# Performance work log

Hardware: AMD Instinct MI355X
Metric: run time of the kernel (lower is better)

Reference implementation:

```python
import jax, jax.numpy as jnp
import numpy as np
from jax import lax

CONV_SIZE = 5
MORPH_SIZE = 5
TH1_INIT = 0.5
STEP = 0.0005
LO, HI = 0.84, 0.86


def _maxpool(a):
    p = MORPH_SIZE // 2
    return lax.reduce_window(
        a, -jnp.inf, lax.max,
        window_dimensions=(1, 1, MORPH_SIZE, MORPH_SIZE),
        window_strides=(1, 1, 1, 1),
        padding=[(0, 0), (0, 0), (p, p), (p, p)])


def setup_inputs() -> dict:
    key = jax.random.key(0)
    k1, _ = jax.random.split(key)
    x = jax.random.uniform(k1, (8, 4, 1024, 1024), dtype=jnp.float32)
    blur_k = jnp.full((1, 1, CONV_SIZE, CONV_SIZE), 1.0 / CONV_SIZE ** 2, dtype=jnp.float32)
    return {"x": x, "blur_k": blur_k}


def reference(x, blur_k):
    N, c, h, w = x.shape
    xi = x.reshape(N * c, 1, h, w)
    out = lax.conv_general_dilated(
        xi, blur_k, window_strides=(1, 1), padding='SAME',
        dimension_numbers=('NCHW', 'OIHW', 'NCHW')).reshape(N, c, h, w)

    # iterative mean-based threshold (quantile) search, same as the torch while-loops
    out_c = lax.stop_gradient(out)

    def frac_above(th):
        return jnp.mean(jnp.where(out_c > th, 1.0, 0.0))

    th = jnp.float32(TH1_INIT)
    th = lax.while_loop(lambda t: frac_above(t) < LO, lambda t: t - STEP, th)
    th = lax.while_loop(lambda t: frac_above(t) > HI, lambda t: t + STEP, th)

    thr = jnp.where(out > th, 1.0, 0.0)
    # morphological close: max-pool then min-pool (min = -maxpool(-x))
    closed = -_maxpool(-_maxpool(thr))
    return closed  # torch casts to float64; kept float32 (see notes)
```

## Files before the change

kernel.cpp:

```cpp
#include <hip/hip_runtime.h>


#define K_STEPS 1024
#define LO_COUNT 28185723u
#define R_TILE 8
#define PT_ROWS 16

#define OFF_HIST 4096
#define OFF_KQ   16384

__global__ void k_init(const float* __restrict__ bk, unsigned int* __restrict__ U,
                       unsigned int* __restrict__ hist) {
    __shared__ float Tsh[K_STEPS];
    int t = threadIdx.x;
    for (int i = t; i < K_STEPS + 1; i += 256) hist[i] = 0u;
    if (t == 0) {
        float th = 0.5f;
        for (int k = 0; k < K_STEPS; k++) { Tsh[k] = th; th = th - 0.0005f; }
    }
    __syncthreads();
    double c = (double)bk[0] * (1.0 / 8388608.0);
    for (int k = t; k < K_STEPS; k += 256) {
        double T = (double)Tsh[k];
        unsigned int u;
        if (T < 0.0) {
            u = 0u;
        } else {
            u = (unsigned int)(floor(T / c) + 1.0);
            while (u > 0u && (double)(u - 1u) * c > T) u--;
            while (!((double)u * c > T)) u++;
        }
        U[k] = u;
    }
}

__device__ __forceinline__ uint4 cvt4(float4 f) {
    return make_uint4((unsigned int)(f.x * 8388608.0f),
                      (unsigned int)(f.y * 8388608.0f),
                      (unsigned int)(f.z * 8388608.0f),
                      (unsigned int)(f.w * 8388608.0f));
}

__device__ __forceinline__ int find_ki(const unsigned int* __restrict__ Us,
                                       float U0f, unsigned int s) {
    float g = (U0f - (float)s) * 9.5367432e-6f;
    int lo = (int)g - 2;
    lo = max(0, min(1019, lo));
    unsigned int a0 = Us[lo], a1 = Us[lo + 1], a2 = Us[lo + 2], a3 = Us[lo + 3];
    return lo + (int)(s < a0) + (int)(s < a1) + (int)(s < a2) + (int)(s < a3);
}

__global__ __launch_bounds__(256, 4) void
k_pass1(const float4* __restrict__ x4, const unsigned int* __restrict__ Ug,
        unsigned int* __restrict__ hist, unsigned short* __restrict__ kq16) {
    __shared__ unsigned int Us[K_STEPS];
    __shared__ unsigned int lh[K_STEPS + 1];
    int tid = threadIdx.x;
    int p = blockIdx.y, y0 = blockIdx.x * R_TILE;
    for (int i = tid; i < K_STEPS; i += 256) Us[i] = Ug[i];
    for (int i = tid; i < K_STEPS + 1; i += 256) lh[i] = 0u;
    __syncthreads();
    float U0f = (float)Us[0];

    const float4* pf = x4 + (size_t)p * 262144;
    int tB = (tid < 255) ? tid + 1 : 0;
    const uint4 z4 = make_uint4(0u, 0u, 0u, 0u);

    uint4 A[5], B[5];
    #pragma unroll
    for (int i = 0; i < 5; i++) {
        int yy = y0 - 2 + i;
        int yc = min(max(yy, 0), 1023);
        float4 fa = pf[yc * 256 + tid];
        float4 fb = pf[yc * 256 + tB];
        bool v = (unsigned)yy < 1024u;
        A[i] = v ? cvt4(fa) : z4;
        B[i] = v ? cvt4(fb) : z4;
    }

    unsigned int cnt0 = 0;
    #pragma unroll
    for (int iy = 0; iy < R_TILE; iy++) {
        int y = y0 + iy;

        float4 Na, Nb;
        if (iy < R_TILE - 1) {
            int yn = min(y + 3, 1023);
            Na = pf[yn * 256 + tid];
            Nb = pf[yn * 256 + tB];
        }

        unsigned int s0 = A[0].x + A[1].x + A[2].x + A[3].x + A[4].x;
        unsigned int s1 = A[0].y + A[1].y + A[2].y + A[3].y + A[4].y;
        unsigned int s2 = A[0].z + A[1].z + A[2].z + A[3].z + A[4].z;
        unsigned int s3 = A[0].w + A[1].w + A[2].w + A[3].w + A[4].w;
        unsigned int s4 = B[0].x + B[1].x + B[2].x + B[3].x + B[4].x;
        unsigned int s5 = B[0].y + B[1].y + B[2].y + B[3].y + B[4].y;
        unsigned int s6 = B[0].z + B[1].z + B[2].z + B[3].z + B[4].z;
        unsigned int s7 = B[0].w + B[1].w + B[2].w + B[3].w + B[4].w;

        unsigned int m123 = s1 + s2 + s3;
        unsigned int h45  = s4 + s5;
        unsigned int v0, v1, v2, v3;
        if (tid != 255) {
            v0 = s0 + m123 + s4;
            v1 = m123 + h45;
            v2 = s2 + s3 + h45 + s6;
            v3 = s3 + h45 + s6 + s7;
        } else {
            v0 = s0 + m123;
            v1 = m123;
            v2 = h45 + s6;
            v3 = h45 + s6 + s7;
        }

        int k0 = find_ki(Us, U0f, v0);
        int k1 = find_ki(Us, U0f, v1);
        int k2 = find_ki(Us, U0f, v2);
        int k3 = find_ki(Us, U0f, v3);
        cnt0 += (unsigned)(k0 == 0) + (unsigned)(k1 == 0)
              + (unsigned)(k2 == 0) + (unsigned)(k3 == 0);
        if (k0 > 0) atomicAdd(&lh[k0], 1u);
        if (k1 > 0) atomicAdd(&lh[k1], 1u);
        if (k2 > 0) atomicAdd(&lh[k2], 1u);
        if (k3 > 0) atomicAdd(&lh[k3], 1u);

        unsigned short pa = (unsigned short)(min(k0, 255) | (min(k1, 255) << 8));
        unsigned short pb = (unsigned short)(min(k2, 255) | (min(k3, 255) << 8));
        size_t rb = ((size_t)p * 1024 + (size_t)y) * 512;
        kq16[rb + 2 * tid + 1] = pa;
        kq16[rb + ((tid < 255) ? (2 * tid + 2) : 0)] = pb;

        if (iy < R_TILE - 1) {
            bool vn = (y + 3) < 1024;
            A[0] = A[1]; A[1] = A[2]; A[2] = A[3]; A[3] = A[4];
            A[4] = vn ? cvt4(Na) : z4;
            B[0] = B[1]; B[1] = B[2]; B[2] = B[3]; B[3] = B[4];
            B[4] = vn ? cvt4(Nb) : z4;
        }
    }

    #pragma unroll
    for (int d = 32; d > 0; d >>= 1) cnt0 += __shfl_down(cnt0, d);
    if ((tid & 63) == 0 && cnt0) atomicAdd(&lh[0], cnt0);
    __syncthreads();
    for (int i = tid; i < K_STEPS + 1; i += 256) {
        unsigned int c = lh[i];
        if (c) atomicAdd(&hist[i], c);
    }
}

__global__ __launch_bounds__(256) void
k_post(const unsigned char* __restrict__ kqb, const unsigned int* __restrict__ hist,
       float* __restrict__ out) {
    __shared__ unsigned long long Tt[24 * 16];
    __shared__ unsigned long long Vv[20 * 16];
    __shared__ unsigned long long Dd[20 * 16];
    __shared__ unsigned long long Ww[16 * 16];
    __shared__ unsigned long long Ff[16 * 16];
    __shared__ int ksS;

    int tid = threadIdx.x;
    int p = blockIdx.y, y0 = blockIdx.x * PT_ROWS;

    if (tid < 64) {
        int lane = tid;
        unsigned int h[16], s = 0;
        #pragma unroll
        for (int i = 0; i < 16; i++) { h[i] = hist[lane * 16 + i]; s += h[i]; }
        unsigned int inc = s;
        #pragma unroll
        for (int d = 1; d < 64; d <<= 1) {
            unsigned int t = __shfl_up(inc, d);
            if (lane >= d) inc += t;
        }
        unsigned int excl = inc - s;
        bool cross = (excl < LO_COUNT) && (excl + s >= LO_COUNT);
        unsigned long long m = __ballot(cross);
        if (m) {
            int cl = __ffsll((long long)m) - 1;
            if (lane == cl) {
                unsigned int c = excl; int ks = K_STEPS - 1;
                for (int i = 0; i < 16; i++) { c += h[i]; if (c >= LO_COUNT) { ks = lane * 16 + i; break; } }
                ksS = ks;
            }
        } else if (lane == 0) ksS = K_STEPS - 1;
    }
    __syncthreads();
    int ks = ksS;

    const unsigned char* kp = kqb + (size_t)p * 1048576;
    unsigned short* Tt16 = (unsigned short*)Tt;
    #pragma unroll
    for (int i = 0; i < 6; i++) {
        int ch = tid + 256 * i;
        int r = ch >> 6, cc = ch & 63;
        int pr = y0 - 4 + r;
        unsigned int m = 0u;
        if ((unsigned)pr < 1024u) {
            uint4 q = ((const uint4*)(kp + (size_t)pr * 1024))[cc];
            unsigned int wv;
            wv = q.x;
            m |= (unsigned)((wv & 0xffu) <= (unsigned)ks)
               | ((unsigned)(((wv >> 8) & 0xffu) <= (unsigned)ks) << 1)
               | ((unsigned)(((wv >> 16) & 0xffu) <= (unsigned)ks) << 2)
               | ((unsigned)((wv >> 24) <= (unsigned)ks) << 3);
            wv = q.y;
            m |= ((unsigned)((wv & 0xffu) <= (unsigned)ks) << 4)
               | ((unsigned)(((wv >> 8) & 0xffu) <= (unsigned)ks) << 5)
               | ((unsigned)(((wv >> 16) & 0xffu) <= (unsigned)ks) << 6)
               | ((unsigned)((wv >> 24) <= (unsigned)ks) << 7);
            wv = q.z;
            m |= ((unsigned)((wv & 0xffu) <= (unsigned)ks) << 8)
               | ((unsigned)(((wv >> 8) & 0xffu) <= (unsigned)ks) << 9)
               | ((unsigned)(((wv >> 16) & 0xffu) <= (unsigned)ks) << 10)
               | ((unsigned)((wv >> 24) <= (unsigned)ks) << 11);
            wv = q.w;
            m |= ((unsigned)((wv & 0xffu) <= (unsigned)ks) << 12)
               | ((unsigned)(((wv >> 8) & 0xffu) <= (unsigned)ks) << 13)
               | ((unsigned)(((wv >> 16) & 0xffu) <= (unsigned)ks) << 14)
               | ((unsigned)((wv >> 24) <= (unsigned)ks) << 15);
        }
        Tt16[ch] = (unsigned short)m;
    }
    __syncthreads();

    for (int i = tid; i < 320; i += 256) {
        int vr = i >> 4, wc = i & 15;
        int b = vr * 16 + wc;
        Vv[i] = Tt[b] | Tt[b + 16] | Tt[b + 32] | Tt[b + 48] | Tt[b + 64];
    }
    __syncthreads();

    for (int i = tid; i < 320; i += 256) {
        int vr = i >> 4, wc = i & 15;
        int pr = y0 - 2 + vr;
        if ((unsigned)pr >= 1024u) { Dd[i] = ~0ull; continue; }
        unsigned long long Vc = Vv[i];
        unsigned long long Vl = (wc > 0)  ? Vv[i - 1] : 0ull;
        unsigned long long Vr = (wc < 15) ? Vv[i + 1] : 0ull;
        Dd[i] = Vc
            | (Vc << 1) | (Vl >> 63)
            | (Vc << 2) | (Vl >> 62)
            | (Vc >> 1) | (Vr << 63)
            | (Vc >> 2) | (Vr << 62);
    }
    __syncthreads();

    {
        int wr = tid >> 4, wc = tid & 15;
        int b = wr * 16 + wc;
        Ww[tid] = Dd[b] & Dd[b + 16] & Dd[b + 32] & Dd[b + 48] & Dd[b + 64];
    }
    __syncthreads();

    {
        int wc = tid & 15;
        unsigned long long Wc = Ww[tid];
        unsigned long long Wl = (wc > 0)  ? Ww[tid - 1] : ~0ull;
        unsigned long long Wr = (wc < 15) ? Ww[tid + 1] : ~0ull;
        Ff[tid] = Wc
            & ((Wc << 1) | (Wl >> 63))
            & ((Wc << 2) | (Wl >> 62))
            & ((Wc >> 1) | (Wr << 63))
            & ((Wc >> 2) | (Wr << 62));
    }
    __syncthreads();

    for (int i = 0; i < PT_ROWS; i++) {
        unsigned long long wd = Ff[i * 16 + (tid >> 4)];
        int sh = (tid & 15) * 4;
        float4 f;
        f.x = (float)((wd >> sh) & 1ull);
        f.y = (float)((wd >> (sh + 1)) & 1ull);
        f.z = (float)((wd >> (sh + 2)) & 1ull);
        f.w = (float)((wd >> (sh + 3)) & 1ull);
        ((float4*)(out + (size_t)p * 1048576 + (size_t)(y0 + i) * 1024))[tid] = f;
    }
}

extern "C" void kernel_launch(void* const* d_in, const int* in_sizes, int n_in,
                              void* d_out, int out_size, void* d_ws, size_t ws_size,
                              hipStream_t stream) {
    const float4* x4 = (const float4*)d_in[0];
    const float*  bk = (const float*)d_in[1];
    float* out = (float*)d_out;

    char* ws = (char*)d_ws;
    unsigned int*   Ug   = (unsigned int*)(ws);
    unsigned int*   hist = (unsigned int*)(ws + OFF_HIST);
    unsigned short* kq16 = (unsigned short*)(ws + OFF_KQ);
    const unsigned char* kqb = (const unsigned char*)(ws + OFF_KQ);

    k_init<<<1, 256, 0, stream>>>(bk, Ug, hist);

    dim3 g1(1024 / R_TILE, 32);
    k_pass1<<<g1, 256, 0, stream>>>(x4, Ug, hist, kq16);

    dim3 g2(1024 / PT_ROWS, 32);
    k_post<<<g2, 256, 0, stream>>>(kqb, hist, out);
}
```

Baseline: 309.0 us.

## Fuse threshold-table init into pass1, use sliding column sums and packed stores

Removes the separate single-block init kernel: the threshold table is now a compile-time constant, every pass1 block computes its own integer threshold table, and the histogram is cleared with a memset. Pass1 switches from recomputing five-row column sums each row to a running sum that adds the incoming row and subtracts the outgoing one, doubles the rows per block, and narrows the lookup window from four to three entries. Output stores are packed into 32-bit writes with a lane shuffle. The cost is redundant double-precision table setup in every block and extra row reloads for the subtracted rows.

```diff
diff --git a/kernel.cpp b/kernel.cpp
--- a/kernel.cpp
+++ b/kernel.cpp
@@ -3,36 +3,20 @@
 
 #define K_STEPS 1024
 #define LO_COUNT 28185723u
-#define R_TILE 8
+#define R_TILE 16
 #define PT_ROWS 16
 
 #define OFF_HIST 4096
 #define OFF_KQ   16384
 
-__global__ void k_init(const float* __restrict__ bk, unsigned int* __restrict__ U,
-                       unsigned int* __restrict__ hist) {
-    __shared__ float Tsh[K_STEPS];
-    int t = threadIdx.x;
-    for (int i = t; i < K_STEPS + 1; i += 256) hist[i] = 0u;
-    if (t == 0) {
-        float th = 0.5f;
-        for (int k = 0; k < K_STEPS; k++) { Tsh[k] = th; th = th - 0.0005f; }
-    }
-    __syncthreads();
-    double c = (double)bk[0] * (1.0 / 8388608.0);
-    for (int k = t; k < K_STEPS; k += 256) {
-        double T = (double)Tsh[k];
-        unsigned int u;
-        if (T < 0.0) {
-            u = 0u;
-        } else {
-            u = (unsigned int)(floor(T / c) + 1.0);
-            while (u > 0u && (double)(u - 1u) * c > T) u--;
-            while (!((double)u * c > T)) u++;
-        }
-        U[k] = u;
-    }
-}
+struct TTable { float v[K_STEPS]; };
+static constexpr TTable make_T() {
+    TTable t{};
+    float th = 0.5f;
+    for (int k = 0; k < K_STEPS; k++) { t.v[k] = th; th = th - 0.0005f; }
+    return t;
+}
+__device__ constexpr TTable Tc = make_T();
 
 __device__ __forceinline__ uint4 cvt4(float4 f) {
     return make_uint4((unsigned int)(f.x * 8388608.0f),
@@ -44,20 +28,35 @@
 __device__ __forceinline__ int find_ki(const unsigned int* __restrict__ Us,
                                        float U0f, unsigned int s) {
     float g = (U0f - (float)s) * 9.5367432e-6f;
-    int lo = (int)g - 2;
-    lo = max(0, min(1019, lo));
-    unsigned int a0 = Us[lo], a1 = Us[lo + 1], a2 = Us[lo + 2], a3 = Us[lo + 3];
-    return lo + (int)(s < a0) + (int)(s < a1) + (int)(s < a2) + (int)(s < a3);
+    int lo = (int)g;
+    lo = max(0, min(1021, lo));
+    unsigned int a0 = Us[lo], a1 = Us[lo + 1], a2 = Us[lo + 2];
+    return lo + (int)(s < a0) + (int)(s < a1) + (int)(s < a2);
 }
 
 __global__ __launch_bounds__(256, 4) void
-k_pass1(const float4* __restrict__ x4, const unsigned int* __restrict__ Ug,
+k_pass1(const float4* __restrict__ x4, const float* __restrict__ bk,
         unsigned int* __restrict__ hist, unsigned short* __restrict__ kq16) {
     __shared__ unsigned int Us[K_STEPS];
     __shared__ unsigned int lh[K_STEPS + 1];
     int tid = threadIdx.x;
     int p = blockIdx.y, y0 = blockIdx.x * R_TILE;
-    for (int i = tid; i < K_STEPS; i += 256) Us[i] = Ug[i];
+
+    {
+        double c = (double)bk[0] * (1.0 / 8388608.0);
+        #pragma unroll
+        for (int i = 0; i < 4; i++) {
+            int k = tid + 256 * i;
+            double T = (double)Tc.v[k];
+            unsigned int u = 0u;
+            if (T >= 0.0) {
+                u = (unsigned int)(floor(T / c) + 1.0);
+                while (u > 0u && (double)(u - 1u) * c > T) u--;
+                while (!((double)u * c > T)) u++;
+            }
+            Us[k] = u;
+        }
+    }
     for (int i = tid; i < K_STEPS + 1; i += 256) lh[i] = 0u;
     __syncthreads();
     float U0f = (float)Us[0];
@@ -66,52 +65,54 @@
     int tB = (tid < 255) ? tid + 1 : 0;
     const uint4 z4 = make_uint4(0u, 0u, 0u, 0u);
 
-    uint4 A[5], B[5];
-    #pragma unroll
-    for (int i = 0; i < 5; i++) {
-        int yy = y0 - 2 + i;
-        int yc = min(max(yy, 0), 1023);
-        float4 fa = pf[yc * 256 + tid];
-        float4 fb = pf[yc * 256 + tB];
-        bool v = (unsigned)yy < 1024u;
-        A[i] = v ? cvt4(fa) : z4;
-        B[i] = v ? cvt4(fb) : z4;
+    unsigned int cs0 = 0, cs1 = 0, cs2 = 0, cs3 = 0,
+                 cs4 = 0, cs5 = 0, cs6 = 0, cs7 = 0;
+    {
+        float4 ra[5], rb[5];
+        #pragma unroll
+        for (int i = 0; i < 5; i++) {
+            int yy = y0 - 2 + i, yc = min(max(yy, 0), 1023);
+            ra[i] = pf[yc * 256 + tid];
+            rb[i] = pf[yc * 256 + tB];
+        }
+        #pragma unroll
+        for (int i = 0; i < 5; i++) {
+            bool v = (unsigned)(y0 - 2 + i) < 1024u;
+            uint4 a = v ? cvt4(ra[i]) : z4;
+            uint4 b = v ? cvt4(rb[i]) : z4;
+            cs0 += a.x; cs1 += a.y; cs2 += a.z; cs3 += a.w;
+            cs4 += b.x; cs5 += b.y; cs6 += b.z; cs7 += b.w;
+        }
+    }
+    float4 N0a, N0b, N1a, N1b, O0a, O0b, O1a, O1b;
+    {
+        int yn0 = min(y0 + 3, 1023), yn1 = min(y0 + 4, 1023);
+        int yo0 = max(y0 - 2, 0),    yo1 = max(y0 - 1, 0);
+        N0a = pf[yn0 * 256 + tid]; N0b = pf[yn0 * 256 + tB];
+        N1a = pf[yn1 * 256 + tid]; N1b = pf[yn1 * 256 + tB];
+        O0a = pf[yo0 * 256 + tid]; O0b = pf[yo0 * 256 + tB];
+        O1a = pf[yo1 * 256 + tid]; O1b = pf[yo1 * 256 + tB];
     }
 
     unsigned int cnt0 = 0;
-    #pragma unroll
+    int wlane = tid & 63;
+    #pragma unroll 4
     for (int iy = 0; iy < R_TILE; iy++) {
         int y = y0 + iy;
 
-        float4 Na, Nb;
-        if (iy < R_TILE - 1) {
-            int yn = min(y + 3, 1023);
-            Na = pf[yn * 256 + tid];
-            Nb = pf[yn * 256 + tB];
-        }
-
-        unsigned int s0 = A[0].x + A[1].x + A[2].x + A[3].x + A[4].x;
-        unsigned int s1 = A[0].y + A[1].y + A[2].y + A[3].y + A[4].y;
-        unsigned int s2 = A[0].z + A[1].z + A[2].z + A[3].z + A[4].z;
-        unsigned int s3 = A[0].w + A[1].w + A[2].w + A[3].w + A[4].w;
-        unsigned int s4 = B[0].x + B[1].x + B[2].x + B[3].x + B[4].x;
-        unsigned int s5 = B[0].y + B[1].y + B[2].y + B[3].y + B[4].y;
-        unsigned int s6 = B[0].z + B[1].z + B[2].z + B[3].z + B[4].z;
-        unsigned int s7 = B[0].w + B[1].w + B[2].w + B[3].w + B[4].w;
-
-        unsigned int m123 = s1 + s2 + s3;
-        unsigned int h45  = s4 + s5;
+        unsigned int m123 = cs1 + cs2 + cs3;
+        unsigned int h45  = cs4 + cs5;
         unsigned int v0, v1, v2, v3;
         if (tid != 255) {
-            v0 = s0 + m123 + s4;
+            v0 = cs0 + m123 + cs4;
             v1 = m123 + h45;
-            v2 = s2 + s3 + h45 + s6;
-            v3 = s3 + h45 + s6 + s7;
+            v2 = cs2 + cs3 + h45 + cs6;
+            v3 = cs3 + h45 + cs6 + cs7;
         } else {
-            v0 = s0 + m123;
+            v0 = cs0 + m123;
             v1 = m123;
-            v2 = h45 + s6;
-            v3 = h45 + s6 + s7;
+            v2 = h45 + cs6;
+            v3 = h45 + cs6 + cs7;
         }
 
         int k0 = find_ki(Us, U0f, v0);
@@ -125,18 +126,35 @@
         if (k2 > 0) atomicAdd(&lh[k2], 1u);
         if (k3 > 0) atomicAdd(&lh[k3], 1u);
 
-        unsigned short pa = (unsigned short)(min(k0, 255) | (min(k1, 255) << 8));
-        unsigned short pb = (unsigned short)(min(k2, 255) | (min(k3, 255) << 8));
+        unsigned int pa = (unsigned)min(k0, 255) | ((unsigned)min(k1, 255) << 8);
+        unsigned int pb = (unsigned)min(k2, 255) | ((unsigned)min(k3, 255) << 8);
+        unsigned int paN = __shfl_down(pa, 1);
         size_t rb = ((size_t)p * 1024 + (size_t)y) * 512;
-        kq16[rb + 2 * tid + 1] = pa;
-        kq16[rb + ((tid < 255) ? (2 * tid + 2) : 0)] = pb;
-
-        if (iy < R_TILE - 1) {
-            bool vn = (y + 3) < 1024;
-            A[0] = A[1]; A[1] = A[2]; A[2] = A[3]; A[3] = A[4];
-            A[4] = vn ? cvt4(Na) : z4;
-            B[0] = B[1]; B[1] = B[2]; B[2] = B[3]; B[3] = B[4];
-            B[4] = vn ? cvt4(Nb) : z4;
+        if (wlane < 63) {
+            ((unsigned int*)(kq16 + rb))[tid + 1] = pb | (paN << 16);
+        } else {
+            kq16[rb + ((tid < 255) ? (unsigned)(2 * tid + 2) : 0u)] =
+                (unsigned short)pb;
+        }
+        if (wlane == 0) kq16[rb + 2 * tid + 1] = (unsigned short)pa;
+
+        {
+            bool vn = (unsigned)(y + 3) < 1024u;
+            bool vo = (y - 2) >= 0;
+            uint4 na = vn ? cvt4(N0a) : z4;
+            uint4 nb = vn ? cvt4(N0b) : z4;
+            uint4 oa = vo ? cvt4(O0a) : z4;
+            uint4 ob = vo ? cvt4(O0b) : z4;
+            cs0 += na.x - oa.x; cs1 += na.y - oa.y;
+            cs2 += na.z - oa.z; cs3 += na.w - oa.w;
+            cs4 += nb.x - ob.x; cs5 += nb.y - ob.y;
+            cs6 += nb.z - ob.z; cs7 += nb.w - ob.w;
+        }
+        N0a = N1a; N0b = N1b; O0a = O1a; O0b = O1b;
+        {
+            int yn = min(y + 5, 1023);
+            N1a = pf[yn * 256 + tid]; N1b = pf[yn * 256 + tB];
+            O1a = pf[y * 256 + tid];  O1b = pf[y * 256 + tB];
         }
     }
 
@@ -287,15 +305,14 @@
     float* out = (float*)d_out;
 
     char* ws = (char*)d_ws;
-    unsigned int*   Ug   = (unsigned int*)(ws);
     unsigned int*   hist = (unsigned int*)(ws + OFF_HIST);
     unsigned short* kq16 = (unsigned short*)(ws + OFF_KQ);
     const unsigned char* kqb = (const unsigned char*)(ws + OFF_KQ);
 
-    k_init<<<1, 256, 0, stream>>>(bk, Ug, hist);
+    hipMemsetAsync(hist, 0, (K_STEPS + 1) * sizeof(unsigned int), stream);
 
     dim3 g1(1024 / R_TILE, 32);
-    k_pass1<<<g1, 256, 0, stream>>>(x4, Ug, hist, kq16);
+    k_pass1<<<g1, 256, 0, stream>>>(x4, bk, hist, kq16);
 
     dim3 g2(1024 / PT_ROWS, 32);
     k_post<<<g2, 256, 0, stream>>>(kqb, hist, out);
```

Result: faster. 282.2 us (-8.7%).
